# Optimization experiments

Hardware: AMD Instinct MI355X
Metric: run time of the kernel (lower is better)

Reference implementation:

```python
import jax, jax.numpy as jnp
import numpy as np

BS, NS, D, H = 4, 1024, 2048, 16
DH = D // H
SCALE = DH ** -0.5
MASK_BIAS = -1e9


def setup_inputs() -> dict:
    key = jax.random.key(0)
    k1, k2, k3, k4, k5 = jax.random.split(key, 5)
    x = jax.random.normal(k1, (BS, NS, D), dtype=jnp.float32)
    attention_ids = jax.random.randint(k2, (BS, NS), 0, 2, dtype=jnp.int32)
    # torch.nn.Linear weights: [out_features, in_features]
    w_in = jax.random.normal(k3, (3 * D, D), dtype=jnp.float32) * (D ** -0.5)
    w_out = jax.random.normal(k4, (D, D), dtype=jnp.float32) * (D ** -0.5)
    b_out = jax.random.normal(k5, (D,), dtype=jnp.float32) * 0.02
    return {"x": x, "attention_ids": attention_ids, "w_in": w_in,
            "w_out": w_out, "b_out": b_out}


def reference(x, attention_ids, w_in, w_out, b_out):
    bs, ns, _ = x.shape
    qkv = jnp.einsum('bsd,ed->bse', x, w_in)            # [bs, ns, 3*D]
    qkv = qkv.reshape(bs, ns, 3, H, DH).transpose(2, 0, 3, 1, 4)
    q, k, v = qkv[0], qkv[1], qkv[2]                     # [bs, H, ns, DH]
    attn = jnp.einsum('bhqd,bhkd->bhqk', q, k)           # [bs, H, ns, ns]
    # NOTE: mask bias added BEFORE the scale multiply, as in the source.
    bias = (attention_ids.astype(attn.dtype) * MASK_BIAS)[:, None, None, :]
    attn = jax.nn.softmax((attn + bias) * SCALE, axis=-1)
    out = jnp.einsum('bhqk,bhkd->bhqd', attn, v)         # [bs, H, ns, DH]
    out = out.transpose(0, 2, 1, 3).reshape(bs, ns, D)
    return jnp.einsum('bsd,ed->bse', out, w_out) + b_out
```

## Files before the change

kernel.cpp:

```cpp
#include <hip/hip_runtime.h>
#include <hip/hip_bf16.h>
#include <stdint.h>

typedef __bf16 bf16;
typedef __bf16 bf16x8 __attribute__((ext_vector_type(8)));
typedef __bf16 bf16x4 __attribute__((ext_vector_type(4)));
typedef float floatx4 __attribute__((ext_vector_type(4)));

#define NSEQ   1024
#define DM     2048
#define NH     16
#define DHD    128
#define E3     6144
#define SCALE_F 0.08838834764831845f
#define MBIAS_S (-1.0e9f * SCALE_F)
#define NEG_HUGE (-3.0e38f)
#define DEFER_THR 8.0f

static __device__ __forceinline__ floatx4 mfma16(bf16x8 a, bf16x8 b, floatx4 c) {
  return __builtin_amdgcn_mfma_f32_16x16x32_bf16(a, b, c, 0, 0, 0);
}

static __device__ __forceinline__ void load_lds16(const bf16* g, bf16* l) {
  __builtin_amdgcn_global_load_lds(
      (__attribute__((address_space(1))) const void*)g,
      (__attribute__((address_space(3))) void*)l, 16, 0, 0);
}

__global__ __launch_bounds__(256) void cast3_kernel(
    const float* __restrict__ x, const float* __restrict__ wi,
    const float* __restrict__ wo, bf16* __restrict__ xb,
    bf16* __restrict__ wib, bf16* __restrict__ wob) {
  const int blk = blockIdx.x;
  const float* src;
  bf16* dst;
  int base;
  if (blk < 8192)       { src = x;  dst = xb;  base = blk; }
  else if (blk < 20480) { src = wi; dst = wib; base = blk - 8192; }
  else                  { src = wo; dst = wob; base = blk - 20480; }
  const int i = base * 256 + threadIdx.x;
  float4 v = ((const float4*)src)[i];
  bf16x4 o;
  o[0] = (bf16)v.x; o[1] = (bf16)v.y; o[2] = (bf16)v.z; o[3] = (bf16)v.w;
  ((bf16x4*)dst)[i] = o;
}

template <typename OutT>
__global__ __launch_bounds__(256) void gemm_bt_kernel(
    const bf16* __restrict__ A, const bf16* __restrict__ B,
    OutT* __restrict__ C, const float* __restrict__ bias,
    int N, int K) {
  __shared__ bf16 As[128 * 32];
  __shared__ bf16 Bs[128 * 32];
  const int ntn = N >> 7;
  const int tm = blockIdx.x / ntn;
  const int tn = blockIdx.x - tm * ntn;
  const int tid = threadIdx.x;
  const int w = tid >> 6;
  const int lane = tid & 63;
  const int lq = lane & 15;
  const int lg = lane >> 4;
  const int wr = w >> 1;
  const int wc = w & 1;

  const bf16* Ag = A + (size_t)(tm * 128) * K;
  const bf16* Bg = B + (size_t)(tn * 128) * K;
  const int c0 = tid, c1 = tid + 256;
  const int r0 = c0 >> 2, o0 = (c0 & 3) * 8;
  const int r1 = c1 >> 2, o1 = (c1 & 3) * 8;
  bf16* lA0 = As + w * 512;
  bf16* lA1 = As + w * 512 + 2048;
  bf16* lB0 = Bs + w * 512;
  bf16* lB1 = Bs + w * 512 + 2048;

  floatx4 acc[4][4] = {};

  for (int k0 = 0; k0 < K; k0 += 32) {
    load_lds16(Ag + (size_t)r0 * K + k0 + o0, lA0);
    load_lds16(Ag + (size_t)r1 * K + k0 + o1, lA1);
    load_lds16(Bg + (size_t)r0 * K + k0 + o0, lB0);
    load_lds16(Bg + (size_t)r1 * K + k0 + o1, lB1);
    __syncthreads();
    bf16x8 af[4], bfr[4];
#pragma unroll
    for (int m = 0; m < 4; m++)
      af[m] = *(const bf16x8*)(As + (wr * 64 + m * 16 + lq) * 32 + lg * 8);
#pragma unroll
    for (int n = 0; n < 4; n++)
      bfr[n] = *(const bf16x8*)(Bs + (wc * 64 + n * 16 + lq) * 32 + lg * 8);
#pragma unroll
    for (int m = 0; m < 4; m++)
#pragma unroll
      for (int n = 0; n < 4; n++)
        acc[m][n] = mfma16(af[m], bfr[n], acc[m][n]);
    __syncthreads();
  }

#pragma unroll
  for (int n = 0; n < 4; n++) {
    const int ccol = tn * 128 + wc * 64 + n * 16 + lq;
    const float bv = bias ? bias[ccol] : 0.f;
#pragma unroll
    for (int m = 0; m < 4; m++) {
      const size_t rbase = (size_t)(tm * 128 + wr * 64 + m * 16 + lg * 4);
#pragma unroll
      for (int r = 0; r < 4; r++)
        C[(rbase + r) * N + ccol] = (OutT)(acc[m][n][r] + bv);
    }
  }
}

__global__ __launch_bounds__(256) void vtrans_kernel(const bf16* __restrict__ qkv,
                                                     bf16* __restrict__ vt) {
  const int bid = blockIdx.x;
  const int sblk = bid & 7;
  const int h = (bid >> 3) & 15;
  const int b = bid >> 7;
  const int t = threadIdx.x;
  const int dhb = (t & 7) | (((t >> 6) & 1) << 3);
  const int sb  = ((t >> 3) & 7) | (((t >> 7) & 1) << 3);
  const int s0 = sblk * 128 + sb * 8;
  const int dh0 = dhb * 8;
  const bf16* src = qkv + (size_t)(b * NSEQ + s0) * E3 + 2 * DM + h * DHD + dh0;
  bf16x8 r[8];
#pragma unroll
  for (int i = 0; i < 8; i++) r[i] = *(const bf16x8*)(src + (size_t)i * E3);
  bf16* dst = vt + ((size_t)(b * NH + h) * DHD + dh0) * NSEQ + s0;
#pragma unroll
  for (int j = 0; j < 8; j++) {
    bf16x8 o;
#pragma unroll
    for (int i = 0; i < 8; i++) o[i] = r[i][j];
    *(bf16x8*)(dst + (size_t)j * NSEQ) = o;
  }
}

__global__ __launch_bounds__(256) void attn_kernel(
    const bf16* __restrict__ qkv, const bf16* __restrict__ vt,
    const int* __restrict__ ids, bf16* __restrict__ ao) {
  __shared__ bf16 Ksh[2][64 * 128];
  __shared__ bf16 Vsh[2][128 * 64];
  __shared__ bf16 plds[4][16][72];
  const int bid = blockIdx.x;
  const int qt = bid & 15;
  const int h = (bid >> 4) & 15;
  const int b = bid >> 8;
  const int tid = threadIdx.x;
  const int w = tid >> 6;
  const int lane = tid & 63;
  const int lq = lane & 15;
  const int lg = lane >> 4;
  const int q0 = qt * 64 + w * 16;
  const int swz = (lq & 7) << 4;

  const int krow0 = w * 16 + (lane >> 4);
  const int kc = lane & 15;
  const int vrow0 = w * 32 + (lane >> 3);
  const int vc = lane & 7;
  const int vr7 = (lane >> 3) & 7;

  const bf16* kg = qkv + DM + h * DHD;
  const bf16* vg = vt + (size_t)(b * NH + h) * DHD * NSEQ;

  auto stage = [&](int buf, int k0) {
#pragma unroll
    for (int i = 0; i < 4; i++) {
      const int kr = krow0 + i * 4;
      load_lds16(kg + (size_t)(b * NSEQ + k0 + kr) * E3 + ((kc ^ (kr & 7)) * 8),
                 &Ksh[buf][(w * 16 + i * 4) * 128]);
    }
#pragma unroll
    for (int i = 0; i < 4; i++) {
      const int vr = vrow0 + i * 8;
      load_lds16(vg + (size_t)vr * NSEQ + k0 + ((vc ^ vr7) * 8),
                 &Vsh[buf][(w * 32 + i * 8) * 64]);
    }
  };

  bf16x8 qf[4];
  const bf16* qb = qkv + (size_t)(b * NSEQ + q0 + lq) * E3 + h * DHD + lg * 8;
#pragma unroll
  for (int kk = 0; kk < 4; kk++) qf[kk] = *(const bf16x8*)(qb + kk * 32);

  floatx4 acc[8] = {};
  float M[4], L[4];
#pragma unroll
  for (int r = 0; r < 4; r++) { M[r] = NEG_HUGE; L[r] = 0.f; }

  bf16 (*pw)[72] = plds[w];
  const int* idb = ids + b * NSEQ;

  stage(0, 0);
  __syncthreads();
  int cur = 0;

  for (int t = 0; t < 16; t++) {
    const int k0 = t * 64;
    if (t < 15) stage(cur ^ 1, k0 + 64);

    const bf16* Kc = Ksh[cur];
    floatx4 s[4] = {};
    __builtin_amdgcn_s_setprio(1);
#pragma unroll
    for (int n = 0; n < 4; n++) {
      const int krow = n * 16 + lq;
#pragma unroll
      for (int kk = 0; kk < 4; kk++) {
        bf16x8 kf = *(const bf16x8*)(Kc + krow * 128 +
                                     (((kk * 64 + lg * 16) ^ swz) >> 1));
        s[n] = mfma16(qf[kk], kf, s[n]);
      }
    }
    __builtin_amdgcn_s_setprio(0);
    float sa[4][4], pm[4];
#pragma unroll
    for (int r = 0; r < 4; r++) pm[r] = NEG_HUGE;
#pragma unroll
    for (int n = 0; n < 4; n++) {
      const float bv = idb[k0 + n * 16 + lq] ? MBIAS_S : 0.f;
#pragma unroll
      for (int r = 0; r < 4; r++) {
        sa[n][r] = s[n][r] * SCALE_F + bv;
        pm[r] = fmaxf(pm[r], sa[n][r]);
      }
    }
#pragma unroll
    for (int m = 1; m <= 8; m <<= 1)
#pragma unroll
      for (int r = 0; r < 4; r++) pm[r] = fmaxf(pm[r], __shfl_xor(pm[r], m, 64));

    int grew = 0;
#pragma unroll
    for (int r = 0; r < 4; r++) grew |= (pm[r] > M[r] + DEFER_THR) ? 1 : 0;
    const bool full = __any(grew);
    float corr[4];
    if (full) {
#pragma unroll
      for (int r = 0; r < 4; r++) {
        const float mn = fmaxf(M[r], pm[r]);
        corr[r] = __expf(M[r] - mn);
        M[r] = mn;
      }
    }
    float rs[4] = {0.f, 0.f, 0.f, 0.f};
#pragma unroll
    for (int n = 0; n < 4; n++)
#pragma unroll
      for (int r = 0; r < 4; r++) {
        const float p = __expf(sa[n][r] - M[r]);
        sa[n][r] = p;
        rs[r] += p;
      }
#pragma unroll
    for (int m = 1; m <= 8; m <<= 1)
#pragma unroll
      for (int r = 0; r < 4; r++) rs[r] += __shfl_xor(rs[r], m, 64);
    if (full) {
#pragma unroll
      for (int r = 0; r < 4; r++) L[r] = L[r] * corr[r] + rs[r];
#pragma unroll
      for (int n8 = 0; n8 < 8; n8++)
#pragma unroll
        for (int r = 0; r < 4; r++) acc[n8][r] *= corr[r];
    } else {
#pragma unroll
      for (int r = 0; r < 4; r++) L[r] += rs[r];
    }
#pragma unroll
    for (int n = 0; n < 4; n++)
#pragma unroll
      for (int r = 0; r < 4; r++) pw[lg * 4 + r][n * 16 + lq] = (bf16)sa[n][r];
    bf16x8 pf0 = *(const bf16x8*)(&pw[lq][lg * 8]);
    bf16x8 pf1 = *(const bf16x8*)(&pw[lq][32 + lg * 8]);
    const bf16* Vc = Vsh[cur];
    __builtin_amdgcn_s_setprio(1);
#pragma unroll
    for (int n8 = 0; n8 < 8; n8++) {
      const int vrow = n8 * 16 + lq;
      bf16x8 v0 = *(const bf16x8*)(Vc + vrow * 64 + (((lg * 16) ^ swz) >> 1));
      bf16x8 v1 = *(const bf16x8*)(Vc + vrow * 64 + (((64 + lg * 16) ^ swz) >> 1));
      acc[n8] = mfma16(pf0, v0, acc[n8]);
      acc[n8] = mfma16(pf1, v1, acc[n8]);
    }
    __builtin_amdgcn_s_setprio(0);
    __syncthreads();
    cur ^= 1;
  }

  float inv[4];
#pragma unroll
  for (int r = 0; r < 4; r++) inv[r] = 1.f / L[r];
  bf16* aob = ao + (size_t)(b * NSEQ + q0 + lg * 4) * DM + h * DHD + lq;
#pragma unroll
  for (int n8 = 0; n8 < 8; n8++)
#pragma unroll
    for (int r = 0; r < 4; r++)
      aob[(size_t)r * DM + n8 * 16] = (bf16)(acc[n8][r] * inv[r]);
}

extern "C" void kernel_launch(void* const* d_in, const int* in_sizes, int n_in,
                              void* d_out, int out_size, void* d_ws, size_t ws_size,
                              hipStream_t stream) {
  const float* x     = (const float*)d_in[0];
  const int*   ids   = (const int*)d_in[1];
  const float* w_in  = (const float*)d_in[2];
  const float* w_out = (const float*)d_in[3];
  const float* b_out = (const float*)d_in[4];
  float* out = (float*)d_out;

  bf16* ws  = (bf16*)d_ws;
  bf16* xb  = ws;
  bf16* wib = xb  + (size_t)4096 * 2048;
  bf16* wob = wib + (size_t)6144 * 2048;
  bf16* qkv = wob + (size_t)2048 * 2048;
  bf16* vtb = qkv + (size_t)4096 * 6144;
  bf16* aob = vtb + (size_t)4 * 16 * 128 * 1024;

  cast3_kernel<<<24576, 256, 0, stream>>>(x, w_in, w_out, xb, wib, wob);
  gemm_bt_kernel<bf16><<<32 * 48, 256, 0, stream>>>(xb, wib, qkv, nullptr, 6144, 2048);
  vtrans_kernel<<<512, 256, 0, stream>>>(qkv, vtb);
  attn_kernel<<<1024, 256, 0, stream>>>(qkv, vtb, ids, aob);
  gemm_bt_kernel<float><<<32 * 16, 256, 0, stream>>>(aob, wob, out, b_out, 2048, 2048);
}
```

Measured before the change: 321.4 us.

## Rewrite GEMM with triple-buffered LDS pipeline, larger tiles, and swizzled reads

Replaces the simple GEMM with a 512-thread kernel computing 128x256 tiles over a K step of 64. Operand tiles are triple-buffered in LDS and prefetched two iterations ahead, with partial vmcnt waits and one barrier per iteration instead of two. LDS rows use an XOR swizzle to avoid bank conflicts, and s_setprio is raised around the MFMA block. The aim is to overlap global-to-LDS loads with MFMA work and raise arithmetic intensity. In exchange it uses more LDS and launches fewer blocks (768 and 256), which may reduce occupancy or leave the out-projection GEMM with too little parallelism.

```diff
diff --git a/kernel.cpp b/kernel.cpp
--- a/kernel.cpp
+++ b/kernel.cpp
@@ -26,6 +26,8 @@
       (__attribute__((address_space(1))) const void*)g,
       (__attribute__((address_space(3))) void*)l, 16, 0, 0);
 }
+
+#define SCHED0 __builtin_amdgcn_sched_barrier(0)
 
 __global__ __launch_bounds__(256) void cast3_kernel(
     const float* __restrict__ x, const float* __restrict__ wi,
@@ -46,66 +48,97 @@
 }
 
 template <typename OutT>
-__global__ __launch_bounds__(256) void gemm_bt_kernel(
+__global__ __launch_bounds__(512) void gemmA_bt_kernel(
     const bf16* __restrict__ A, const bf16* __restrict__ B,
     OutT* __restrict__ C, const float* __restrict__ bias,
     int N, int K) {
-  __shared__ bf16 As[128 * 32];
-  __shared__ bf16 Bs[128 * 32];
-  const int ntn = N >> 7;
+  __shared__ __align__(16) bf16 Al[3][2][128 * 32];
+  __shared__ __align__(16) bf16 Bl[3][2][256 * 32];
+  const int NT = K >> 6;
+  const int ntn = N >> 8;
   const int tm = blockIdx.x / ntn;
   const int tn = blockIdx.x - tm * ntn;
   const int tid = threadIdx.x;
-  const int w = tid >> 6;
-  const int lane = tid & 63;
-  const int lq = lane & 15;
-  const int lg = lane >> 4;
-  const int wr = w >> 1;
-  const int wc = w & 1;
+  const int w = tid >> 6, lane = tid & 63;
+  const int lq = lane & 15, lg = lane >> 4;
+  const int wr = w >> 2, wc = w & 3;
+  const int sub = lane >> 2;
+  const int cpl = (lane & 3) ^ ((lane >> 3) & 3);
+  const int scp8 = (lg ^ ((lq >> 1) & 3)) << 3;
 
   const bf16* Ag = A + (size_t)(tm * 128) * K;
-  const bf16* Bg = B + (size_t)(tn * 128) * K;
-  const int c0 = tid, c1 = tid + 256;
-  const int r0 = c0 >> 2, o0 = (c0 & 3) * 8;
-  const int r1 = c1 >> 2, o1 = (c1 & 3) * 8;
-  bf16* lA0 = As + w * 512;
-  bf16* lA1 = As + w * 512 + 2048;
-  bf16* lB0 = Bs + w * 512;
-  bf16* lB1 = Bs + w * 512 + 2048;
+  const bf16* Bg = B + (size_t)(tn * 256) * K;
+
+  auto STAGE = [&](int buf, int kcol) {
+#pragma unroll
+    for (int kh = 0; kh < 2; kh++)
+      load_lds16(Ag + (size_t)(w * 16 + sub) * K + kcol + kh * 32 + cpl * 8,
+                 Al[buf][kh] + (w * 16) * 32);
+#pragma unroll
+    for (int kh = 0; kh < 2; kh++)
+#pragma unroll
+      for (int j = 0; j < 2; j++) {
+        const int r0 = w * 32 + j * 16;
+        load_lds16(Bg + (size_t)(r0 + sub) * K + kcol + kh * 32 + cpl * 8,
+                   Bl[buf][kh] + r0 * 32);
+      }
+  };
+  auto RD = [&](const bf16* slot, int rbase) -> bf16x8 {
+    return *(const bf16x8*)(slot + (rbase + lq) * 32 + scp8);
+  };
 
   floatx4 acc[4][4] = {};
 
-  for (int k0 = 0; k0 < K; k0 += 32) {
-    load_lds16(Ag + (size_t)r0 * K + k0 + o0, lA0);
-    load_lds16(Ag + (size_t)r1 * K + k0 + o1, lA1);
-    load_lds16(Bg + (size_t)r0 * K + k0 + o0, lB0);
-    load_lds16(Bg + (size_t)r1 * K + k0 + o1, lB1);
-    __syncthreads();
-    bf16x8 af[4], bfr[4];
+  STAGE(0, 0);
+  STAGE(1, 64);
+  asm volatile("s_waitcnt vmcnt(6)" ::: "memory");
+  SCHED0;
+  __builtin_amdgcn_s_barrier();
+  SCHED0;
+
+  int b0 = 0, b1 = 1, b2 = 2;
+  for (int t = 0; t < NT; ++t) {
+    const int kc2 = ((t + 2 < NT) ? t + 2 : NT - 1) << 6;
+    STAGE(b2, kc2);
+    bf16x8 af0[4], af1[4], bq0[4], bq1[4];
+#pragma unroll
+    for (int m = 0; m < 4; m++) {
+      af0[m] = RD(Al[b0][0], wr * 64 + m * 16);
+      af1[m] = RD(Al[b0][1], wr * 64 + m * 16);
+    }
+#pragma unroll
+    for (int n = 0; n < 4; n++) {
+      bq0[n] = RD(Bl[b0][0], wc * 64 + n * 16);
+      bq1[n] = RD(Bl[b0][1], wc * 64 + n * 16);
+    }
+    __builtin_amdgcn_s_setprio(1);
 #pragma unroll
     for (int m = 0; m < 4; m++)
-      af[m] = *(const bf16x8*)(As + (wr * 64 + m * 16 + lq) * 32 + lg * 8);
-#pragma unroll
-    for (int n = 0; n < 4; n++)
-      bfr[n] = *(const bf16x8*)(Bs + (wc * 64 + n * 16 + lq) * 32 + lg * 8);
+#pragma unroll
+      for (int n = 0; n < 4; n++)
+        acc[m][n] = mfma16(af0[m], bq0[n], acc[m][n]);
 #pragma unroll
     for (int m = 0; m < 4; m++)
 #pragma unroll
       for (int n = 0; n < 4; n++)
-        acc[m][n] = mfma16(af[m], bfr[n], acc[m][n]);
-    __syncthreads();
+        acc[m][n] = mfma16(af1[m], bq1[n], acc[m][n]);
+    __builtin_amdgcn_s_setprio(0);
+    asm volatile("s_waitcnt vmcnt(6)" ::: "memory");
+    SCHED0; __builtin_amdgcn_s_barrier(); SCHED0;
+    const int tmp = b0; b0 = b1; b1 = b2; b2 = tmp;
   }
-
-#pragma unroll
-  for (int n = 0; n < 4; n++) {
-    const int ccol = tn * 128 + wc * 64 + n * 16 + lq;
-    const float bv = bias ? bias[ccol] : 0.f;
+  asm volatile("s_waitcnt vmcnt(0)" ::: "memory");
+
+#pragma unroll
+  for (int ni = 0; ni < 4; ni++) {
+    const int col = tn * 256 + wc * 64 + ni * 16 + lq;
+    const float bv = bias ? bias[col] : 0.f;
 #pragma unroll
     for (int m = 0; m < 4; m++) {
-      const size_t rbase = (size_t)(tm * 128 + wr * 64 + m * 16 + lg * 4);
+      const size_t rb = (size_t)(tm * 128 + wr * 64 + m * 16 + lg * 4);
 #pragma unroll
       for (int r = 0; r < 4; r++)
-        C[(rbase + r) * N + ccol] = (OutT)(acc[m][n][r] + bv);
+        C[(rb + r) * N + col] = (OutT)(acc[m][ni][r] + bv);
     }
   }
 }
@@ -317,8 +350,8 @@
   bf16* aob = vtb + (size_t)4 * 16 * 128 * 1024;
 
   cast3_kernel<<<24576, 256, 0, stream>>>(x, w_in, w_out, xb, wib, wob);
-  gemm_bt_kernel<bf16><<<32 * 48, 256, 0, stream>>>(xb, wib, qkv, nullptr, 6144, 2048);
+  gemmA_bt_kernel<bf16><<<768, 512, 0, stream>>>(xb, wib, qkv, nullptr, 6144, 2048);
   vtrans_kernel<<<512, 256, 0, stream>>>(qkv, vtb);
   attn_kernel<<<1024, 256, 0, stream>>>(qkv, vtb, ids, aob);
-  gemm_bt_kernel<float><<<32 * 16, 256, 0, stream>>>(aob, wob, out, b_out, 2048, 2048);
-}
+  gemmA_bt_kernel<float><<<256, 512, 0, stream>>>(aob, wob, out, b_out, 2048, 2048);
+}
```

New measurement: 318.6 us. No clear change (-0.9%).
